# Performance work log

Measured on AMD Instinct MI355X. Metric: run time of the kernel, lower is better.

## Reference

```python
import jax, jax.numpy as jnp
import numpy as np


def _mlp(x, W1, b1, W2, b2):
    # x: (B, M, T); torch MLPLayer: transpose(1,2) -> Linear -> Linear -> LeakyReLU -> transpose back
    h = jnp.einsum('bmt,hm->bht', x, W1) + b1[None, :, None]   # (B, H, T)
    y = jnp.einsum('bht,oh->bot', h, W2) + b2[None, :, None]   # (B, M, T)
    return jax.nn.leaky_relu(y, negative_slope=0.01)


def _calc_attn(q, k, v):
    # q: (B, M, Tq), k: (B, M, Tk), v: (B, M, Tk)
    Tq = q.shape[-1]
    qk = jnp.einsum('bmq,bmk->bqk', q, k)                       # (B, Tq, Tk)
    eye = jnp.eye(Tq, dtype=qk.dtype)                           # broadcasts: (Tq,Tq) or (1,1)
    logits = jnp.exp(qk - qk * eye / jnp.sqrt(jnp.asarray(Tq, qk.dtype)))
    scores = jax.nn.softmax(logits, axis=-1)
    return jnp.einsum('bqk,bmk->bmq', scores, v)                # (B, M, Tq)


def setup_inputs() -> dict:
    key = jax.random.key(0)
    B, M, T, H = 16, 128, 2048, 512
    ks = jax.random.split(key, 14)
    s = 0.02
    inp = {
        'pattern': jax.random.normal(ks[0], (B, M, T), jnp.float32),
        'value': jax.random.normal(ks[1], (B, M, T), jnp.float32),
        'kernel_size': 33,
    }
    names = ['q', 'k', 'o']
    for i, n in enumerate(names):
        inp['W%s1' % n] = jax.random.normal(ks[2 + 4 * i], (H, M), jnp.float32) * s
        inp['b%s1' % n] = jax.random.normal(ks[3 + 4 * i], (H,), jnp.float32) * s
        inp['W%s2' % n] = jax.random.normal(ks[4 + 4 * i], (M, H), jnp.float32) * s
        inp['b%s2' % n] = jax.random.normal(ks[5 + 4 * i], (M,), jnp.float32) * s
    return inp


def reference(pattern, value, kernel_size, Wq1, bq1, Wq2, bq2, Wk1, bk1, Wk2, bk2, Wo1, bo1, Wo2, bo2):
    query = _mlp(pattern, Wq1, bq1, Wq2, bq2)
    key = _mlp(pattern, Wk1, bk1, Wk2, bk2)
    # full (internal) attention
    attn_in = _calc_attn(query, key, value)                     # (B, M, T)
    rep_in = _mlp(attn_in, Wo1, bo1, Wo2, bo2)
    # windowed (external) attention
    T = query.shape[-1]
    cu = (kernel_size - 1) // 2
    q_w = query[..., T - 1 - cu : T - cu]                       # (B, M, 1)
    k_w = key[..., kernel_size - cu - 1 : T - cu - 2]           # (B, M, T-k-1)
    v_w = value[..., kernel_size : T - 1]                       # (B, M, T-k-1)
    attn_ex = _calc_attn(q_w, k_w, v_w)                         # (B, M, 1)
    rep_ex = _mlp(attn_ex, Wo1, bo1, Wo2, bo2)
    return jnp.concatenate([rep_in, rep_ex], axis=-1)           # (B, M, T+1)
```

## Files before the change

kernel.cpp:

```cpp
#include <hip/hip_runtime.h>
#include <hip/hip_bf16.h>
#include <math.h>

#define B_    16
#define M_    128
#define T_    2048
#define H_    512
#define TOUT_ 2049

typedef unsigned short u16;
typedef unsigned int   u32;
typedef __bf16 bf16x8 __attribute__((ext_vector_type(8)));
typedef float  f32x16 __attribute__((ext_vector_type(16)));
typedef float  f32x4  __attribute__((ext_vector_type(4)));
typedef u32    u32x4  __attribute__((ext_vector_type(4)));
typedef u32    u32x2  __attribute__((ext_vector_type(2)));

#define A_OFF     0
#define C_OFF     16384
#define MEAN_OFF  16896
#define AQKBF_OFF 19200
#define AOBF_OFF  35584
#define QT_OFF    43776
#define KT_OFF    (43776 + 2097152)
#define VB_OFF    (43776 + 2 * 2097152)

static __device__ __forceinline__ u16 f2bf(float f) {
  u32 u = __float_as_uint(f);
  u = (u + 0x7FFFu + ((u >> 16) & 1u)) >> 16;
  return (u16)u;
}
static __device__ __forceinline__ u32 pk2(float lo, float hi) {
  __hip_bfloat162 h = __float22bfloat162_rn(float2{lo, hi});
  u32 r;
  __builtin_memcpy(&r, &h, 4);
  return r;
}
static __device__ __forceinline__ bf16x8 ldfrag(const u16* p) {
  return __builtin_bit_cast(bf16x8, *(const u32x4*)p);
}
static __device__ __forceinline__ float ex2(float x) {
#if __has_builtin(__builtin_amdgcn_exp2f)
  return __builtin_amdgcn_exp2f(x);
#else
  return exp2f(x);
#endif
}

__global__ __launch_bounds__(128) void fuse_weights_all(
    const float* __restrict__ W1q, const float* __restrict__ b1q,
    const float* __restrict__ W2q, const float* __restrict__ b2q,
    const float* __restrict__ W1k, const float* __restrict__ b1k,
    const float* __restrict__ W2k, const float* __restrict__ b2k,
    const float* __restrict__ W1o, const float* __restrict__ b1o,
    const float* __restrict__ W2o, const float* __restrict__ b2o,
    float* __restrict__ A, float* __restrict__ c,
    u16* __restrict__ Aqk_bf, u16* __restrict__ Ao_bf) {
  __shared__ float w2row[H_];
  int which = blockIdx.x >> 7;
  int o = blockIdx.x & 127;
  const float* W1 = which == 0 ? W1q : which == 1 ? W1k : W1o;
  const float* b1 = which == 0 ? b1q : which == 1 ? b1k : b1o;
  const float* W2 = which == 0 ? W2q : which == 1 ? W2k : W2o;
  const float* b2 = which == 0 ? b2q : which == 1 ? b2k : b2o;
  int m = threadIdx.x;
  for (int h = m; h < H_; h += 128) w2row[h] = W2[o * H_ + h];
  __syncthreads();
  float acc = 0.f;
#pragma unroll 8
  for (int h = 0; h < H_; ++h) acc = fmaf(w2row[h], W1[h * M_ + m], acc);
  u16 ab = f2bf(acc);
  if (which == 0)      Aqk_bf[o * 128 + m] = ab;
  else if (which == 1) Aqk_bf[(128 + o) * 128 + m] = ab;
  else               { Ao_bf[o * 128 + m] = ab; A[o * M_ + m] = acc; }
  if (m < 64) {
    float cc = 0.f;
    for (int h = m; h < H_; h += 64) cc = fmaf(w2row[h], b1[h], cc);
#pragma unroll
    for (int off = 32; off > 0; off >>= 1) cc += __shfl_down(cc, off, 64);
    if (m == 0) c[which * 128 + o] = cc + b2[o];
  }
}

#define XS 68

__global__ __launch_bounds__(256) void prep_kernel(
    const float* __restrict__ pattern, const u16* __restrict__ Aqk_bf,
    const float* __restrict__ cqk, u16* __restrict__ qT, u16* __restrict__ kT,
    const float* __restrict__ value, u16* __restrict__ vb,
    float* __restrict__ meanv) {
  __shared__ alignas(16) float xsf[128 * XS];
  int bx = blockIdx.x;
  int tid = threadIdx.x;

  if (bx >= 512) {
    int bm = bx - 512;
    float* red = xsf;
    const float* row = value + (size_t)bm * T_;
    int i0 = tid * 8;
    float4 a = *(const float4*)(row + i0);
    float4 bq = *(const float4*)(row + i0 + 4);
    u32x4 o = {pk2(a.x, a.y), pk2(a.z, a.w), pk2(bq.x, bq.y), pk2(bq.z, bq.w)};
    *(u32x4*)&vb[(size_t)bm * T_ + i0] = o;
    float vals[8] = {a.x, a.y, a.z, a.w, bq.x, bq.y, bq.z, bq.w};
    float s = 0.f;
#pragma unroll
    for (int j = 0; j < 8; ++j) {
      int idx = i0 + j;
      if (idx >= 33 && idx < T_ - 1) s += vals[j];
    }
    red[tid] = s;
    __syncthreads();
    for (int st = 128; st > 0; st >>= 1) {
      if (tid < st) red[tid] += red[tid + st];
      __syncthreads();
    }
    if (tid == 0) meanv[bm] = red[0] * (1.f / 2014.f);
    return;
  }

  int b = bx >> 5;
  int t0 = (bx & 31) * 64;
  int lane = tid & 63;
  int wv = tid >> 6;
  int l31 = lane & 31;
  int lh8 = (lane >> 5) * 8;

  bf16x8 afr[2][8];
#pragma unroll
  for (int i = 0; i < 2; ++i) {
    const u16* ap = Aqk_bf + ((2 * wv + i) * 32 + l31) * 128 + lh8;
#pragma unroll
    for (int s = 0; s < 8; ++s) afr[i][s] = ldfrag(ap + 16 * s);
  }

#pragma unroll
  for (int rep = 0; rep < 8; ++rep) {
    int m = rep * 16 + (tid >> 4);
    int tc = (tid & 15) * 4;
    float4 v = *(const float4*)&pattern[(size_t)(b * M_ + m) * T_ + t0 + tc];
    *(float4*)&xsf[m * XS + tc] = v;
  }
  __syncthreads();

  bf16x8 bfr[2][8];
#pragma unroll
  for (int tt = 0; tt < 2; ++tt) {
#pragma unroll
    for (int s = 0; s < 8; ++s) {
      float v0 = xsf[(s * 16 + lh8 + 0) * XS + tt * 32 + l31];
      float v1 = xsf[(s * 16 + lh8 + 1) * XS + tt * 32 + l31];
      float v2 = xsf[(s * 16 + lh8 + 2) * XS + tt * 32 + l31];
      float v3 = xsf[(s * 16 + lh8 + 3) * XS + tt * 32 + l31];
      float v4 = xsf[(s * 16 + lh8 + 4) * XS + tt * 32 + l31];
      float v5 = xsf[(s * 16 + lh8 + 5) * XS + tt * 32 + l31];
      float v6 = xsf[(s * 16 + lh8 + 6) * XS + tt * 32 + l31];
      float v7 = xsf[(s * 16 + lh8 + 7) * XS + tt * 32 + l31];
      u32x4 p = {pk2(v0, v1), pk2(v2, v3), pk2(v4, v5), pk2(v6, v7)};
      bfr[tt][s] = __builtin_bit_cast(bf16x8, p);
    }
  }
  __syncthreads();

  u16* obuf = (u16*)xsf;
#pragma unroll
  for (int tt = 0; tt < 2; ++tt) {
#pragma unroll
    for (int i = 0; i < 2; ++i) {
      f32x16 acc;
#pragma unroll
      for (int r = 0; r < 16; ++r) acc[r] = 0.f;
#pragma unroll
      for (int s = 0; s < 8; ++s)
        acc = __builtin_amdgcn_mfma_f32_32x32x16_bf16(afr[i][s], bfr[tt][s], acc, 0, 0, 0);
      int ot = 2 * wv + i;
      int t = tt * 32 + l31;
      float sc = (ot < 4) ? 1.44269504f : 1.0f;
#pragma unroll
      for (int r = 0; r < 16; ++r) {
        int orow = (r & 3) + 8 * (r >> 2) + 4 * (lane >> 5);
        float v = acc[r] + cqk[ot * 32 + orow];
        v = v > 0.f ? v : 0.01f * v;
        obuf[t * 258 + ot * 32 + orow] = f2bf(v * sc);
      }
    }
  }
  __syncthreads();

  const u32* ob32 = (const u32*)obuf;
#pragma unroll
  for (int g = 0; g < 8; ++g) {
    int G = wv * 8 + g;
    int mat = G >> 4;
    int t = (G & 15) * 4 + (lane >> 4);
    int og2 = lane & 15;
    int wbase = t * 129 + mat * 64 + og2 * 4;
    u32x4 vv = {ob32[wbase], ob32[wbase + 1], ob32[wbase + 2], ob32[wbase + 3]};
    u32* dst = (u32*)((mat ? kT : qT) + ((size_t)(b * T_ + t0 + t)) * 128) + og2 * 4;
    *(u32x4*)dst = vv;
  }
}

#define QSTR 136
#define VSTR 136
#define KTILE 128
#define NKT  (T_ / KTILE)
#define CINIT 0.52876637f

__global__ __launch_bounds__(512, 2) void attn_mfma_kernel(
    const u16* __restrict__ qT, const u16* __restrict__ kT,
    const u16* __restrict__ vB, const u16* __restrict__ Ao_bf,
    const float* __restrict__ co, const float* __restrict__ Aofp,
    const float* __restrict__ meanv, float* __restrict__ out) {
  extern __shared__ u16 smem[];
  u16* ks0 = smem;
  u16* ks1 = ks0 + 128 * QSTR;
  u16* vs0 = ks1 + 128 * QSTR;
  u16* vs1 = vs0 + 128 * VSTR;
  float* dls  = (float*)(vs1 + 128 * VSTR);
  float* pbuf = (float*)ks0;
  u16*   ptbuf = vs0;

  int b = blockIdx.y;
  int q0 = blockIdx.x * 128;
  int tid = threadIdx.x;
  int lane = tid & 63;
  int wv = tid >> 6;
  int l31 = lane & 31;
  int h = lane >> 5;
  int lh8 = h * 8;
  int qt = wv & 3;
  int kh = wv >> 2;

  const u16* gkb = kT + (size_t)b * T_ * 128;
  const u16* gvb = vB + (size_t)b * M_ * T_;
  int kr = tid >> 4, kc = (tid & 15) * 8;

  bf16x8 qfrag[8];
  {
    const u16* qrow = qT + (size_t)(b * T_ + q0 + qt * 32 + l31) * 128 + lh8;
#pragma unroll
    for (int s = 0; s < 8; ++s) qfrag[s] = ldfrag(qrow + s * 16);
  }

  u32x4 kreg[4], vreg[4];
#pragma unroll
  for (int it = 0; it < 4; ++it) {
    kreg[it] = *(const u32x4*)&gkb[(size_t)(it * 32 + kr) * 128 + kc];
    vreg[it] = *(const u32x4*)&gvb[(size_t)(it * 32 + kr) * T_ + kc];
  }
#pragma unroll
  for (int it = 0; it < 4; ++it) {
    *(u32x4*)&ks0[(it * 32 + kr) * QSTR + kc] = kreg[it];
    *(u32x4*)&vs0[(it * 32 + kr) * VSTR + kc] = vreg[it];
  }
#pragma unroll
  for (int it = 0; it < 4; ++it) {
    kreg[it] = *(const u32x4*)&gkb[(size_t)(KTILE + it * 32 + kr) * 128 + kc];
    vreg[it] = *(const u32x4*)&gvb[(size_t)(it * 32 + kr) * T_ + KTILE + kc];
  }

  f32x16 pacc[4];
  float den = 0.f;
#pragma unroll
  for (int i = 0; i < 16; ++i) {
    pacc[0][i] = 0.f; pacc[1][i] = 0.f; pacc[2][i] = 0.f; pacc[3][i] = 0.f;
  }

  for (int kt = 0; kt < NKT; ++kt) {
    int k0 = kt * KTILE;
    u16* kcur = (kt & 1) ? ks1 : ks0;
    u16* knxt = (kt & 1) ? ks0 : ks1;
    u16* vcur = (kt & 1) ? vs1 : vs0;
    u16* vnxt = (kt & 1) ? vs0 : vs1;
    __syncthreads();

    f32x16 sacc_a, sacc_b;
#pragma unroll
    for (int i = 0; i < 16; ++i) { sacc_a[i] = CINIT; sacc_b[i] = CINIT; }
    {
      const u16* krowa = &kcur[(kh * 64 + l31) * QSTR + lh8];
      const u16* krowb = krowa + 32 * QSTR;
      __builtin_amdgcn_s_setprio(1);
#pragma unroll
      for (int s = 0; s < 8; ++s) {
        bf16x8 kfa = ldfrag(krowa + s * 16);
        sacc_a = __builtin_amdgcn_mfma_f32_32x32x16_bf16(kfa, qfrag[s], sacc_a, 0, 0, 0);
      }
#pragma unroll
      for (int s = 0; s < 8; ++s) {
        bf16x8 kfb = ldfrag(krowb + s * 16);
        sacc_b = __builtin_amdgcn_mfma_f32_32x32x16_bf16(kfb, qfrag[s], sacc_b, 0, 0, 0);
      }
      __builtin_amdgcn_s_setprio(0);
    }

    if (kt < NKT - 1) {
#pragma unroll
      for (int it = 0; it < 4; ++it) {
        *(u32x4*)&knxt[(it * 32 + kr) * QSTR + kc] = kreg[it];
        *(u32x4*)&vnxt[(it * 32 + kr) * VSTR + kc] = vreg[it];
      }
      int kn = (kt + 2 < NKT) ? (kt + 2) * KTILE : (NKT - 1) * KTILE;
#pragma unroll
      for (int it = 0; it < 4; ++it) {
        kreg[it] = *(const u32x4*)&gkb[(size_t)(kn + it * 32 + kr) * 128 + kc];
        vreg[it] = *(const u32x4*)&gvb[(size_t)(it * 32 + kr) * T_ + kn + kc];
      }
    }

    if (k0 + kh * 64 == q0 + qt * 32) {
#pragma unroll
      for (int r = 0; r < 16; ++r) {
        int row = (r & 3) + 8 * (r >> 2) + 4 * h;
        if (row == l31) sacc_a[r] = fmaf(sacc_a[r], 0.97790291f, 0.01168420f);
      }
    } else if (k0 + kh * 64 + 32 == q0 + qt * 32) {
#pragma unroll
      for (int r = 0; r < 16; ++r) {
        int row = (r & 3) + 8 * (r >> 2) + 4 * h;
        if (row == l31) sacc_b[r] = fmaf(sacc_b[r], 0.97790291f, 0.01168420f);
      }
    }

    {
      float w[16];
#pragma unroll
      for (int r = 0; r < 16; ++r) w[r] = ex2(ex2(sacc_a[r]));
      float d0 = (w[0] + w[1]) + (w[2] + w[3]);
      float d1 = (w[4] + w[5]) + (w[6] + w[7]);
      float d2 = (w[8] + w[9]) + (w[10] + w[11]);
      float d3 = (w[12] + w[13]) + (w[14] + w[15]);
      den += (d0 + d1) + (d2 + d3);
      u32 p00 = pk2(w[0], w[1]),  p01 = pk2(w[2], w[3]);
      u32 p10 = pk2(w[4], w[5]),  p11 = pk2(w[6], w[7]);
      u32 p20 = pk2(w[8], w[9]),  p21 = pk2(w[10], w[11]);
      u32 p30 = pk2(w[12], w[13]), p31 = pk2(w[14], w[15]);
      u32 e0 = __shfl_xor(h ? p00 : p10, 32, 64);
      u32 e1 = __shfl_xor(h ? p01 : p11, 32, 64);
      u32 e2 = __shfl_xor(h ? p20 : p30, 32, 64);
      u32 e3 = __shfl_xor(h ? p21 : p31, 32, 64);
      u32x4 f0 = h ? u32x4{e0, e1, p10, p11} : u32x4{p00, p01, e0, e1};
      u32x4 f1 = h ? u32x4{e2, e3, p30, p31} : u32x4{p20, p21, e2, e3};
      bf16x8 bw0 = __builtin_bit_cast(bf16x8, f0);
      bf16x8 bw1 = __builtin_bit_cast(bf16x8, f1);
      __builtin_amdgcn_s_setprio(1);
#pragma unroll
      for (int mt = 0; mt < 4; ++mt) {
        const u16* vrow = &vcur[(mt * 32 + l31) * VSTR + kh * 64 + lh8];
        bf16x8 vf0 = ldfrag(vrow);
        bf16x8 vf1 = ldfrag(vrow + 16);
        pacc[mt] = __builtin_amdgcn_mfma_f32_32x32x16_bf16(vf0, bw0, pacc[mt], 0, 0, 0);
        pacc[mt] = __builtin_amdgcn_mfma_f32_32x32x16_bf16(vf1, bw1, pacc[mt], 0, 0, 0);
      }
      __builtin_amdgcn_s_setprio(0);
    }
    {
      float w[16];
#pragma unroll
      for (int r = 0; r < 16; ++r) w[r] = ex2(ex2(sacc_b[r]));
      float d0 = (w[0] + w[1]) + (w[2] + w[3]);
      float d1 = (w[4] + w[5]) + (w[6] + w[7]);
      float d2 = (w[8] + w[9]) + (w[10] + w[11]);
      float d3 = (w[12] + w[13]) + (w[14] + w[15]);
      den += (d0 + d1) + (d2 + d3);
      u32 p00 = pk2(w[0], w[1]),  p01 = pk2(w[2], w[3]);
      u32 p10 = pk2(w[4], w[5]),  p11 = pk2(w[6], w[7]);
      u32 p20 = pk2(w[8], w[9]),  p21 = pk2(w[10], w[11]);
      u32 p30 = pk2(w[12], w[13]), p31 = pk2(w[14], w[15]);
      u32 e0 = __shfl_xor(h ? p00 : p10, 32, 64);
      u32 e1 = __shfl_xor(h ? p01 : p11, 32, 64);
      u32 e2 = __shfl_xor(h ? p20 : p30, 32, 64);
      u32 e3 = __shfl_xor(h ? p21 : p31, 32, 64);
      u32x4 f0 = h ? u32x4{e0, e1, p10, p11} : u32x4{p00, p01, e0, e1};
      u32x4 f1 = h ? u32x4{e2, e3, p30, p31} : u32x4{p20, p21, e2, e3};
      bf16x8 bw2 = __builtin_bit_cast(bf16x8, f0);
      bf16x8 bw3 = __builtin_bit_cast(bf16x8, f1);
      __builtin_amdgcn_s_setprio(1);
#pragma unroll
      for (int mt = 0; mt < 4; ++mt) {
        const u16* vrow = &vcur[(mt * 32 + l31) * VSTR + kh * 64 + 32 + lh8];
        bf16x8 vf2 = ldfrag(vrow);
        bf16x8 vf3 = ldfrag(vrow + 16);
        pacc[mt] = __builtin_amdgcn_mfma_f32_32x32x16_bf16(vf2, bw2, pacc[mt], 0, 0, 0);
        pacc[mt] = __builtin_amdgcn_mfma_f32_32x32x16_bf16(vf3, bw3, pacc[mt], 0, 0, 0);
      }
      __builtin_amdgcn_s_setprio(0);
    }
  }

  float dq = den + __shfl_xor(den, 32, 64);

  __syncthreads();

  if (kh == 1) {
#pragma unroll
    for (int mt = 0; mt < 4; ++mt) {
      float* pb = &pbuf[((size_t)(qt * 4 + mt) * 64 + lane) * 16];
#pragma unroll
      for (int g = 0; g < 4; ++g) {
        f32x4 v = {pacc[mt][4 * g], pacc[mt][4 * g + 1],
                   pacc[mt][4 * g + 2], pacc[mt][4 * g + 3]};
        *(f32x4*)(pb + 4 * g) = v;
      }
    }
    if (lane < 32) dls[qt * 32 + lane] = dq;
  }
  __syncthreads();

  if (kh == 0) {
    float rden = 1.f / (dq + dls[qt * 32 + l31]);
#pragma unroll
    for (int mt = 0; mt < 4; ++mt) {
      const float* pb = &pbuf[((size_t)(qt * 4 + mt) * 64 + lane) * 16];
#pragma unroll
      for (int g = 0; g < 4; ++g) {
        f32x4 t = *(const f32x4*)(pb + 4 * g);
        float v0 = (pacc[mt][4 * g + 0] + t[0]) * rden;
        float v1 = (pacc[mt][4 * g + 1] + t[1]) * rden;
        float v2 = (pacc[mt][4 * g + 2] + t[2]) * rden;
        float v3 = (pacc[mt][4 * g + 3] + t[3]) * rden;
        int m0 = mt * 32 + 8 * g + 4 * h;
        u32x2 wp = {pk2(v0, v1), pk2(v2, v3)};
        *(u32x2*)&ptbuf[(qt * 32 + l31) * QSTR + m0] = wp;
      }
    }
  }
  __syncthreads();

  bf16x8 aofr[8];
  {
    const u16* ap = Ao_bf + ((wv & 3) * 32 + l31) * 128 + lh8;
#pragma unroll
    for (int s = 0; s < 8; ++s) aofr[s] = ldfrag(ap + 16 * s);
  }
#pragma unroll
  for (int j = 0; j < 2; ++j) {
    int qt2 = kh * 2 + j;
    bf16x8 pfr[8];
    const u16* pp = &ptbuf[(qt2 * 32 + l31) * QSTR + lh8];
#pragma unroll
    for (int s = 0; s < 8; ++s) pfr[s] = ldfrag(pp + 16 * s);
    f32x16 oacc;
#pragma unroll
    for (int r = 0; r < 16; ++r) oacc[r] = 0.f;
#pragma unroll
    for (int s = 0; s < 8; ++s)
      oacc = __builtin_amdgcn_mfma_f32_32x32x16_bf16(aofr[s], pfr[s], oacc, 0, 0, 0);
#pragma unroll
    for (int r = 0; r < 16; ++r) {
      int orow = (wv & 3) * 32 + (r & 3) + 8 * (r >> 2) + 4 * h;
      float v = oacc[r] + co[orow];
      v = v > 0.f ? v : 0.01f * v;
      out[((size_t)(b * M_ + orow)) * TOUT_ + q0 + qt2 * 32 + l31] = v;
    }
  }

  if (blockIdx.x == 0 && tid < 128) {
    float acc = co[tid];
    const float* mv = meanv + b * 128;
    for (int m = 0; m < 128; ++m) acc = fmaf(Aofp[tid * 128 + m], mv[m], acc);
    acc = acc > 0.f ? acc : 0.01f * acc;
    out[((size_t)(b * M_ + tid)) * TOUT_ + 2048] = acc;
  }
}

extern "C" void kernel_launch(void* const* d_in, const int* in_sizes, int n_in,
                              void* d_out, int out_size, void* d_ws, size_t ws_size,
                              hipStream_t stream) {
  (void)in_sizes; (void)n_in; (void)out_size; (void)ws_size;
  const float* pattern = (const float*)d_in[0];
  const float* value   = (const float*)d_in[1];
  const float* Wq1 = (const float*)d_in[3];
  const float* bq1 = (const float*)d_in[4];
  const float* Wq2 = (const float*)d_in[5];
  const float* bq2 = (const float*)d_in[6];
  const float* Wk1 = (const float*)d_in[7];
  const float* bk1 = (const float*)d_in[8];
  const float* Wk2 = (const float*)d_in[9];
  const float* bk2 = (const float*)d_in[10];
  const float* Wo1 = (const float*)d_in[11];
  const float* bo1 = (const float*)d_in[12];
  const float* Wo2 = (const float*)d_in[13];
  const float* bo2 = (const float*)d_in[14];

  float* ws     = (float*)d_ws;
  float* A      = ws + A_OFF;
  float* c      = ws + C_OFF;
  float* meanv  = ws + MEAN_OFF;
  u16*   Aqk_bf = (u16*)(ws + AQKBF_OFF);
  u16*   Ao_bf  = (u16*)(ws + AOBF_OFF);
  u16*   qT     = (u16*)(ws + QT_OFF);
  u16*   kT     = (u16*)(ws + KT_OFF);
  u16*   vB     = (u16*)(ws + VB_OFF);
  float* out    = (float*)d_out;

  fuse_weights_all<<<384, 128, 0, stream>>>(
      Wq1, bq1, Wq2, bq2, Wk1, bk1, Wk2, bk2, Wo1, bo1, Wo2, bo2,
      A, c, Aqk_bf, Ao_bf);

  prep_kernel<<<512 + B_ * M_, 256, 0, stream>>>(
      pattern, Aqk_bf, c, qT, kT, value, vB, meanv);

  size_t lds_bytes = (size_t)(2 * 128 * QSTR + 2 * 128 * VSTR) * 2 + 128 * 4;
  attn_mfma_kernel<<<dim3(T_ / 128, B_), 512, lds_bytes, stream>>>(
      qT, kT, vB, Ao_bf, c + 256, A, meanv, out);
}
```

Measured before the change: 190.1 us.

## Move value conversion into weight-fusion launch and halve prep tile width

The value-to-bf16 conversion and windowed mean reduction move out of prep_kernel into extra blocks of the weight-fusion kernel. Each wave now handles whole rows and reduces with shuffles instead of an LDS tree with repeated barriers. prep_kernel now processes 32 time steps per block, doubling its grid and halving LDS per block, and writes packed bf16 pairs to LDS. The intent is to overlap the independent value pass with the tiny weight fusion and to raise occupancy in the projection kernel. The cost is that each block reuses its loaded A fragments over half as many columns.

Result: no change. 188.9 us (-0.6%).

```diff
diff --git a/kernel.cpp b/kernel.cpp
--- a/kernel.cpp
+++ b/kernel.cpp
@@ -55,15 +55,50 @@
     const float* __restrict__ W1o, const float* __restrict__ b1o,
     const float* __restrict__ W2o, const float* __restrict__ b2o,
     float* __restrict__ A, float* __restrict__ c,
-    u16* __restrict__ Aqk_bf, u16* __restrict__ Ao_bf) {
+    u16* __restrict__ Aqk_bf, u16* __restrict__ Ao_bf,
+    const float* __restrict__ value, u16* __restrict__ vb,
+    float* __restrict__ meanv) {
   __shared__ float w2row[H_];
+  int tid = threadIdx.x;
+
+  if (blockIdx.x >= 384) {
+    int bm0 = (blockIdx.x - 384) * 4;
+    int w = tid >> 6, lane = tid & 63;
+#pragma unroll
+    for (int rr = 0; rr < 2; ++rr) {
+      int bm = bm0 + w * 2 + rr;
+      const float* row = value + (size_t)bm * T_;
+      u16* vrow = vb + (size_t)bm * T_;
+      float s = 0.f;
+#pragma unroll
+      for (int seg = 0; seg < 8; ++seg) {
+        int col = seg * 256 + lane * 4;
+        float4 a = *(const float4*)(row + col);
+        u32x2 o = {pk2(a.x, a.y), pk2(a.z, a.w)};
+        *(u32x2*)&vrow[col] = o;
+        if (col >= 33 && col < T_ - 4) {
+          s += ((a.x + a.y) + (a.z + a.w));
+        } else {
+          if (col + 0 >= 33 && col + 0 < T_ - 1) s += a.x;
+          if (col + 1 >= 33 && col + 1 < T_ - 1) s += a.y;
+          if (col + 2 >= 33 && col + 2 < T_ - 1) s += a.z;
+          if (col + 3 >= 33 && col + 3 < T_ - 1) s += a.w;
+        }
+      }
+#pragma unroll
+      for (int off = 32; off > 0; off >>= 1) s += __shfl_down(s, off, 64);
+      if (lane == 0) meanv[bm] = s * (1.f / 2014.f);
+    }
+    return;
+  }
+
   int which = blockIdx.x >> 7;
   int o = blockIdx.x & 127;
   const float* W1 = which == 0 ? W1q : which == 1 ? W1k : W1o;
   const float* b1 = which == 0 ? b1q : which == 1 ? b1k : b1o;
   const float* W2 = which == 0 ? W2q : which == 1 ? W2k : W2o;
   const float* b2 = which == 0 ? b2q : which == 1 ? b2k : b2o;
-  int m = threadIdx.x;
+  int m = tid;
   for (int h = m; h < H_; h += 128) w2row[h] = W2[o * H_ + h];
   __syncthreads();
   float acc = 0.f;
@@ -82,49 +117,22 @@
   }
 }
 
-#define XS 68
+#define XS2 36
 
 __global__ __launch_bounds__(256) void prep_kernel(
     const float* __restrict__ pattern, const u16* __restrict__ Aqk_bf,
-    const float* __restrict__ cqk, u16* __restrict__ qT, u16* __restrict__ kT,
-    const float* __restrict__ value, u16* __restrict__ vb,
-    float* __restrict__ meanv) {
-  __shared__ alignas(16) float xsf[128 * XS];
+    const float* __restrict__ cqk, u16* __restrict__ qT, u16* __restrict__ kT) {
+  __shared__ alignas(16) float xsf[128 * XS2];
   int bx = blockIdx.x;
   int tid = threadIdx.x;
 
-  if (bx >= 512) {
-    int bm = bx - 512;
-    float* red = xsf;
-    const float* row = value + (size_t)bm * T_;
-    int i0 = tid * 8;
-    float4 a = *(const float4*)(row + i0);
-    float4 bq = *(const float4*)(row + i0 + 4);
-    u32x4 o = {pk2(a.x, a.y), pk2(a.z, a.w), pk2(bq.x, bq.y), pk2(bq.z, bq.w)};
-    *(u32x4*)&vb[(size_t)bm * T_ + i0] = o;
-    float vals[8] = {a.x, a.y, a.z, a.w, bq.x, bq.y, bq.z, bq.w};
-    float s = 0.f;
-#pragma unroll
-    for (int j = 0; j < 8; ++j) {
-      int idx = i0 + j;
-      if (idx >= 33 && idx < T_ - 1) s += vals[j];
-    }
-    red[tid] = s;
-    __syncthreads();
-    for (int st = 128; st > 0; st >>= 1) {
-      if (tid < st) red[tid] += red[tid + st];
-      __syncthreads();
-    }
-    if (tid == 0) meanv[bm] = red[0] * (1.f / 2014.f);
-    return;
-  }
-
-  int b = bx >> 5;
-  int t0 = (bx & 31) * 64;
+  int b = bx >> 6;
+  int t0 = (bx & 63) * 32;
   int lane = tid & 63;
   int wv = tid >> 6;
   int l31 = lane & 31;
-  int lh8 = (lane >> 5) * 8;
+  int h = lane >> 5;
+  int lh8 = h * 8;
 
   bf16x8 afr[2][8];
 #pragma unroll
@@ -134,70 +142,77 @@
     for (int s = 0; s < 8; ++s) afr[i][s] = ldfrag(ap + 16 * s);
   }
 
-#pragma unroll
-  for (int rep = 0; rep < 8; ++rep) {
-    int m = rep * 16 + (tid >> 4);
-    int tc = (tid & 15) * 4;
-    float4 v = *(const float4*)&pattern[(size_t)(b * M_ + m) * T_ + t0 + tc];
-    *(float4*)&xsf[m * XS + tc] = v;
-  }
-  __syncthreads();
-
-  bf16x8 bfr[2][8];
-#pragma unroll
-  for (int tt = 0; tt < 2; ++tt) {
-#pragma unroll
-    for (int s = 0; s < 8; ++s) {
-      float v0 = xsf[(s * 16 + lh8 + 0) * XS + tt * 32 + l31];
-      float v1 = xsf[(s * 16 + lh8 + 1) * XS + tt * 32 + l31];
-      float v2 = xsf[(s * 16 + lh8 + 2) * XS + tt * 32 + l31];
-      float v3 = xsf[(s * 16 + lh8 + 3) * XS + tt * 32 + l31];
-      float v4 = xsf[(s * 16 + lh8 + 4) * XS + tt * 32 + l31];
-      float v5 = xsf[(s * 16 + lh8 + 5) * XS + tt * 32 + l31];
-      float v6 = xsf[(s * 16 + lh8 + 6) * XS + tt * 32 + l31];
-      float v7 = xsf[(s * 16 + lh8 + 7) * XS + tt * 32 + l31];
-      u32x4 p = {pk2(v0, v1), pk2(v2, v3), pk2(v4, v5), pk2(v6, v7)};
-      bfr[tt][s] = __builtin_bit_cast(bf16x8, p);
-    }
+  {
+    int m = tid >> 1;
+    int cb = (tid & 1) * 16;
+#pragma unroll
+    for (int j = 0; j < 4; ++j) {
+      float4 v = *(const float4*)&pattern[(size_t)(b * M_ + m) * T_ + t0 + cb + j * 4];
+      *(float4*)&xsf[m * XS2 + cb + j * 4] = v;
+    }
+  }
+  __syncthreads();
+
+  bf16x8 bfr[8];
+#pragma unroll
+  for (int s = 0; s < 8; ++s) {
+    float v0 = xsf[(s * 16 + lh8 + 0) * XS2 + l31];
+    float v1 = xsf[(s * 16 + lh8 + 1) * XS2 + l31];
+    float v2 = xsf[(s * 16 + lh8 + 2) * XS2 + l31];
+    float v3 = xsf[(s * 16 + lh8 + 3) * XS2 + l31];
+    float v4 = xsf[(s * 16 + lh8 + 4) * XS2 + l31];
+    float v5 = xsf[(s * 16 + lh8 + 5) * XS2 + l31];
+    float v6 = xsf[(s * 16 + lh8 + 6) * XS2 + l31];
+    float v7 = xsf[(s * 16 + lh8 + 7) * XS2 + l31];
+    u32x4 p = {pk2(v0, v1), pk2(v2, v3), pk2(v4, v5), pk2(v6, v7)};
+    bfr[s] = __builtin_bit_cast(bf16x8, p);
   }
   __syncthreads();
 
   u16* obuf = (u16*)xsf;
-#pragma unroll
-  for (int tt = 0; tt < 2; ++tt) {
-#pragma unroll
-    for (int i = 0; i < 2; ++i) {
-      f32x16 acc;
-#pragma unroll
-      for (int r = 0; r < 16; ++r) acc[r] = 0.f;
-#pragma unroll
-      for (int s = 0; s < 8; ++s)
-        acc = __builtin_amdgcn_mfma_f32_32x32x16_bf16(afr[i][s], bfr[tt][s], acc, 0, 0, 0);
-      int ot = 2 * wv + i;
-      int t = tt * 32 + l31;
-      float sc = (ot < 4) ? 1.44269504f : 1.0f;
-#pragma unroll
-      for (int r = 0; r < 16; ++r) {
-        int orow = (r & 3) + 8 * (r >> 2) + 4 * (lane >> 5);
-        float v = acc[r] + cqk[ot * 32 + orow];
-        v = v > 0.f ? v : 0.01f * v;
-        obuf[t * 258 + ot * 32 + orow] = f2bf(v * sc);
-      }
+  u32* ob32w = (u32*)xsf;
+#pragma unroll
+  for (int i = 0; i < 2; ++i) {
+    f32x16 acc;
+#pragma unroll
+    for (int r = 0; r < 16; ++r) acc[r] = 0.f;
+#pragma unroll
+    for (int s = 0; s < 8; ++s)
+      acc = __builtin_amdgcn_mfma_f32_32x32x16_bf16(afr[i][s], bfr[s], acc, 0, 0, 0);
+    int ot = 2 * wv + i;
+    int t = l31;
+    float sc = (ot < 4) ? 1.44269504f : 1.0f;
+#pragma unroll
+    for (int g = 0; g < 4; ++g) {
+      int orow0 = 8 * g + 4 * h;
+      float q0 = acc[4 * g + 0] + cqk[ot * 32 + orow0 + 0];
+      float q1 = acc[4 * g + 1] + cqk[ot * 32 + orow0 + 1];
+      float q2 = acc[4 * g + 2] + cqk[ot * 32 + orow0 + 2];
+      float q3 = acc[4 * g + 3] + cqk[ot * 32 + orow0 + 3];
+      q0 = (q0 > 0.f ? q0 : 0.01f * q0) * sc;
+      q1 = (q1 > 0.f ? q1 : 0.01f * q1) * sc;
+      q2 = (q2 > 0.f ? q2 : 0.01f * q2) * sc;
+      q3 = (q3 > 0.f ? q3 : 0.01f * q3) * sc;
+      int u16i = t * 258 + ot * 32 + orow0;
+      ob32w[(u16i >> 1) + 0] = pk2(q0, q1);
+      ob32w[(u16i >> 1) + 1] = pk2(q2, q3);
     }
   }
   __syncthreads();
 
   const u32* ob32 = (const u32*)obuf;
-#pragma unroll
-  for (int g = 0; g < 8; ++g) {
-    int G = wv * 8 + g;
-    int mat = G >> 4;
-    int t = (G & 15) * 4 + (lane >> 4);
-    int og2 = lane & 15;
-    int wbase = t * 129 + mat * 64 + og2 * 4;
-    u32x4 vv = {ob32[wbase], ob32[wbase + 1], ob32[wbase + 2], ob32[wbase + 3]};
-    u32* dst = (u32*)((mat ? kT : qT) + ((size_t)(b * T_ + t0 + t)) * 128) + og2 * 4;
-    *(u32x4*)dst = vv;
+  {
+    int t = tid >> 3;
+#pragma unroll
+    for (int j = 0; j < 4; ++j) {
+      int qd = (tid & 7) * 4 + j;
+      int base = t * 129 + qd * 4;
+      u32x4 vv = {ob32[base], ob32[base + 1], ob32[base + 2], ob32[base + 3]};
+      int mat = qd >> 4;
+      u32* dst = (u32*)((mat ? kT : qT) + ((size_t)(b * T_ + t0 + t)) * 128)
+               + (qd & 15) * 4;
+      *(u32x4*)dst = vv;
+    }
   }
 }
 
@@ -495,12 +510,11 @@
   u16*   vB     = (u16*)(ws + VB_OFF);
   float* out    = (float*)d_out;
 
-  fuse_weights_all<<<384, 128, 0, stream>>>(
+  fuse_weights_all<<<384 + 512, 128, 0, stream>>>(
       Wq1, bq1, Wq2, bq2, Wk1, bk1, Wk2, bk2, Wo1, bo1, Wo2, bo2,
-      A, c, Aqk_bf, Ao_bf);
-
-  prep_kernel<<<512 + B_ * M_, 256, 0, stream>>>(
-      pattern, Aqk_bf, c, qT, kT, value, vB, meanv);
+      A, c, Aqk_bf, Ao_bf, value, vB, meanv);
+
+  prep_kernel<<<B_ * 64, 256, 0, stream>>>(pattern, Aqk_bf, c, qT, kT);
 
   size_t lds_bytes = (size_t)(2 * 128 * QSTR + 2 * 128 * VSTR) * 2 + 128 * 4;
   attn_mfma_kernel<<<dim3(T_ / 128, B_), 512, lds_bytes, stream>>>(
```
